# Kernel optimization log

Hardware: AMD Instinct MI355X
Metric: run time of the kernel (lower is better)

Reference implementation:

```python
import jax, jax.numpy as jnp
import numpy as np

B, S, D, H = 2, 2048, 1024, 16
HD = D // H  # head_dim = 64

def setup_inputs() -> dict:
    key = jax.random.key(0)
    ks = jax.random.split(key, 5)
    scale = 0.02
    return {
        "x":  jax.random.normal(ks[0], (B, S, D), dtype=jnp.float32),
        "Wq": jax.random.normal(ks[1], (D, D), dtype=jnp.float32) * scale,
        "Wk": jax.random.normal(ks[2], (D, D), dtype=jnp.float32) * scale,
        "Wv": jax.random.normal(ks[3], (D, D), dtype=jnp.float32) * scale,
        "Wo": jax.random.normal(ks[4], (D, D), dtype=jnp.float32) * scale,
    }

def reference(x, Wq, Wk, Wv, Wo):
    b, s, d = x.shape
    # projections (bias-free linear): [b,s,d] @ [d,d]
    q = (x @ Wq).reshape(b, s, H, HD).transpose(0, 2, 1, 3)  # [b,h,s,hd]
    k = (x @ Wk).reshape(b, s, H, HD).transpose(0, 2, 1, 3)
    v = (x @ Wv).reshape(b, s, H, HD).transpose(0, 2, 1, 3)
    scale = jnp.asarray(1.0 / np.sqrt(HD), dtype=x.dtype)
    scores = jnp.einsum('bhqd,bhkd->bhqk', q, k) * scale  # [b,h,s,s]
    causal = jnp.tril(jnp.ones((s, s), dtype=bool))
    scores = jnp.where(causal, scores, jnp.asarray(-jnp.inf, dtype=scores.dtype))
    attn = jax.nn.softmax(scores, axis=-1)
    out = jnp.einsum('bhqk,bhkd->bhqd', attn, v)  # [b,h,s,hd]
    out = out.transpose(0, 2, 1, 3).reshape(b, s, d)
    return out @ Wo
```

## Files before the change

kernel.cpp:

```cpp
#include <hip/hip_runtime.h>
#include <hip/hip_bf16.h>
#include <cstdint>

typedef __bf16 bf16;
typedef bf16 bf16x8 __attribute__((ext_vector_type(8)));
typedef bf16 bf16x4 __attribute__((ext_vector_type(4)));
typedef float f32x4 __attribute__((ext_vector_type(4)));

#define MFMA16(a, b, c) __builtin_amdgcn_mfma_f32_16x16x32_bf16(a, b, c, 0, 0, 0)

struct rawF { f32x4 a, b; };
__device__ inline rawF ldr(const float* p) {
  rawF r; r.a = *(const f32x4*)p; r.b = *(const f32x4*)(p + 4); return r;
}
__device__ inline bf16x8 ldr(const bf16* p) { return *(const bf16x8*)p; }
__device__ inline bf16x8 cv(const rawF& r) {
  bf16x8 o;
#pragma unroll
  for (int i = 0; i < 4; ++i) { o[i] = (bf16)r.a[i]; o[i + 4] = (bf16)r.b[i]; }
  return o;
}
__device__ inline bf16x8 cv(const bf16x8& r) { return r; }
__device__ inline void stC(bf16* C, size_t i, float v) { C[i] = (bf16)v; }
__device__ inline void stC(float* C, size_t i, float v) { C[i] = v; }

__global__ __launch_bounds__(256) void prep_wt(const float* __restrict__ W0,
                                               const float* __restrict__ W1,
                                               const float* __restrict__ W2,
                                               const float* __restrict__ W3,
                                               bf16* __restrict__ Wt, int n) {
  const float* Ws[4] = {W0, W1, W2, W3};
  const float* W = Ws[blockIdx.z];
  bf16* out = Wt + (size_t)blockIdx.z * n * n;
  __shared__ bf16 t[32][33];
  int bx = blockIdx.x * 32, by = blockIdx.y * 32;
  int tx = threadIdx.x & 31, ty = threadIdx.x >> 5;
#pragma unroll
  for (int i = 0; i < 32; i += 8)
    t[ty + i][tx] = (bf16)W[(size_t)(by + ty + i) * n + bx + tx];
  __syncthreads();
#pragma unroll
  for (int i = 0; i < 32; i += 8)
    out[(size_t)(bx + ty + i) * n + by + tx] = t[tx][ty + i];
}

__global__ __launch_bounds__(256) void vtrans(const bf16* __restrict__ V, bf16* __restrict__ Vt) {
  constexpr int Sn = 2048, Dn = 1024;
  __shared__ bf16 t[32][33];
  int s0 = blockIdx.x * 32, hd0 = blockIdx.y * 32, bh = blockIdx.z;
  int b = bh >> 4, h = bh & 15;
  int tx = threadIdx.x & 31, ty = threadIdx.x >> 5;
#pragma unroll
  for (int i = 0; i < 32; i += 8)
    t[ty + i][tx] = V[(size_t)(b * Sn + s0 + ty + i) * Dn + h * 64 + hd0 + tx];
  __syncthreads();
#pragma unroll
  for (int i = 0; i < 32; i += 8)
    Vt[(size_t)bh * 64 * Sn + (size_t)(hd0 + ty + i) * Sn + s0 + tx] = t[tx][ty + i];
}

template <typename TA, typename TC, bool BT>
__global__ __launch_bounds__(256) void gemm3(const TA* __restrict__ A,
                                             const void* __restrict__ B0p,
                                             const void* __restrict__ B1p,
                                             const void* __restrict__ B2p,
                                             TC* __restrict__ C0, TC* __restrict__ C1,
                                             TC* __restrict__ C2, int M, int N, int K, int nblk) {
  constexpr int LDA = 40;
  constexpr int LDB = BT ? 40 : 32;
  __shared__ bf16 As[128 * LDA];
  __shared__ bf16 Bs[128 * LDB];
  int tid = threadIdx.x, wave = tid >> 6, lane = tid & 63;
  int la = lane & 15, quad = lane >> 4;
  int wr = (wave >> 1) * 64, wc = (wave & 1) * 64;
  int by = blockIdx.y;
  int sel = by / nblk;
  int n0 = (by - sel * nblk) * 128;
  const void* Bp = sel == 0 ? B0p : (sel == 1 ? B1p : B2p);
  TC* C = sel == 0 ? C0 : (sel == 1 ? C1 : C2);
  const TA* Ab = A + (size_t)blockIdx.x * 128 * K;
  using TB = typename std::conditional<BT, bf16, float>::type;
  const TB* Bm = (const TB*)Bp;

  int ar[2], ac[2], br[2], bc[2];
#pragma unroll
  for (int p = 0; p < 2; ++p) {
    int li = (tid + p * 256) * 8;
    ar[p] = li >> 5; ac[p] = li & 31;
    if (BT) { br[p] = li >> 5; bc[p] = li & 31; }
    else    { br[p] = li >> 7; bc[p] = li & 127; }
  }

  f32x4 zero = {0.f, 0.f, 0.f, 0.f};
  f32x4 acc[4][4];
#pragma unroll
  for (int i = 0; i < 4; ++i)
#pragma unroll
    for (int j = 0; j < 4; ++j) acc[i][j] = zero;

  decltype(ldr((const TA*)nullptr)) pa[2];
  decltype(ldr((const TB*)nullptr)) pb[2];
#pragma unroll
  for (int p = 0; p < 2; ++p) {
    pa[p] = ldr(&Ab[(size_t)ar[p] * K + ac[p]]);
    if (BT) pb[p] = ldr(&Bm[(size_t)(n0 + br[p]) * K + bc[p]]);
    else    pb[p] = ldr(&Bm[(size_t)br[p] * N + n0 + bc[p]]);
  }

  for (int k0 = 0; k0 < K; k0 += 32) {
#pragma unroll
    for (int p = 0; p < 2; ++p) {
      *(bf16x8*)&As[ar[p] * LDA + ac[p]] = cv(pa[p]);
      if constexpr (BT) {
        *(bf16x8*)&Bs[br[p] * LDB + bc[p]] = cv(pb[p]);
      } else {
        bf16x8 v = cv(pb[p]);
        int kx = br[p] ^ (((bc[p] >> 3) & 3) << 3);
#pragma unroll
        for (int j = 0; j < 8; ++j) Bs[(bc[p] + j) * 32 + kx] = v[j];
      }
    }
    __syncthreads();
    int k1 = k0 + 32;
    if (k1 < K) {
#pragma unroll
      for (int p = 0; p < 2; ++p) {
        pa[p] = ldr(&Ab[(size_t)ar[p] * K + k1 + ac[p]]);
        if (BT) pb[p] = ldr(&Bm[(size_t)(n0 + br[p]) * K + k1 + bc[p]]);
        else    pb[p] = ldr(&Bm[(size_t)(k1 + br[p]) * N + n0 + bc[p]]);
      }
    }
    bf16x8 af[4], bfr[4];
#pragma unroll
    for (int i = 0; i < 4; ++i)
      af[i] = *(const bf16x8*)&As[(wr + i * 16 + la) * LDA + quad * 8];
#pragma unroll
    for (int j = 0; j < 4; ++j) {
      int nr = wc + j * 16 + la;
      if constexpr (BT)
        bfr[j] = *(const bf16x8*)&Bs[nr * LDB + quad * 8];
      else
        bfr[j] = *(const bf16x8*)&Bs[nr * 32 + ((quad * 8) ^ (((nr >> 3) & 3) << 3))];
    }
#pragma unroll
    for (int i = 0; i < 4; ++i)
#pragma unroll
      for (int j = 0; j < 4; ++j) acc[i][j] = MFMA16(af[i], bfr[j], acc[i][j]);
    __syncthreads();
  }
#pragma unroll
  for (int i = 0; i < 4; ++i) {
#pragma unroll
    for (int j = 0; j < 4; ++j) {
      int col = n0 + wc + j * 16 + la;
#pragma unroll
      for (int r = 0; r < 4; ++r) {
        int row = blockIdx.x * 128 + wr + i * 16 + quad * 4 + r;
        stC(C, (size_t)row * N + col, acc[i][j][r]);
      }
    }
  }
}

__global__ __launch_bounds__(256) void flash_attn(const bf16* __restrict__ Q,
                                                  const bf16* __restrict__ Kg,
                                                  const bf16* __restrict__ Vtg,
                                                  bf16* __restrict__ O) {
  constexpr int D = 1024, S = 2048;
  const int LDK = 72, LDP = 72;
  const float MASK = -3.0e4f;
  const float SCL2 = 0.18033688011112042f;
  __shared__ bf16 Ks[64 * 72];
  __shared__ bf16 Vs[64 * 72];
  __shared__ bf16 Ps[4][16 * 72];

  int n = blockIdx.x;
  int bh = n & 31;
  int j5 = n >> 5;
  int j = j5 & 15;
  int qt = (j5 & 16) ? 31 - j : j;
  int b = bh >> 4, h = bh & 15;
  int tid = threadIdx.x, wave = tid >> 6, lane = tid & 63;
  int la = lane & 15, quad = lane >> 4;
  const size_t base = (size_t)b * S * D + (size_t)h * 64;
  const bf16* Qg = Q + base;
  const bf16* Kb = Kg + base;
  const bf16* Vb = Vtg + (size_t)bh * 64 * S;
  int r0 = tid >> 3, c0 = (tid & 7) * 8;

  f32x4 zero = {0.f, 0.f, 0.f, 0.f};

  int q0 = qt * 64;
  int ntiles = qt + 1;

  bf16x8 aq[2];
  {
    int qrow = q0 + wave * 16 + la;
#pragma unroll
    for (int kc = 0; kc < 2; ++kc) {
      bf16x8 t = *(const bf16x8*)&Qg[(size_t)qrow * D + kc * 32 + quad * 8];
#pragma unroll
      for (int i = 0; i < 8; ++i) t[i] = (bf16)((float)t[i] * SCL2);
      aq[kc] = t;
    }
  }

  f32x4 o[4];
#pragma unroll
  for (int nt = 0; nt < 4; ++nt) o[nt] = zero;
  float m_l = MASK, l_l = 0.f;

  bf16x8 kr0 = *(const bf16x8*)&Kb[(size_t)r0 * D + c0];
  bf16x8 kr1 = *(const bf16x8*)&Kb[(size_t)(r0 + 32) * D + c0];
  bf16x8 vr0 = *(const bf16x8*)&Vb[(size_t)r0 * S + c0];
  bf16x8 vr1 = *(const bf16x8*)&Vb[(size_t)(r0 + 32) * S + c0];

  for (int t = 0; t < ntiles; ++t) {
    int kb = t * 64;
    *(bf16x8*)&Ks[r0 * LDK + c0] = kr0;
    *(bf16x8*)&Ks[(r0 + 32) * LDK + c0] = kr1;
    *(bf16x8*)&Vs[r0 * LDK + c0] = vr0;
    *(bf16x8*)&Vs[(r0 + 32) * LDK + c0] = vr1;
    __syncthreads();
    if (t + 1 < ntiles) {
      int kb2 = kb + 64;
      kr0 = *(const bf16x8*)&Kb[(size_t)(kb2 + r0) * D + c0];
      kr1 = *(const bf16x8*)&Kb[(size_t)(kb2 + r0 + 32) * D + c0];
      vr0 = *(const bf16x8*)&Vb[(size_t)r0 * S + kb2 + c0];
      vr1 = *(const bf16x8*)&Vb[(size_t)(r0 + 32) * S + kb2 + c0];
    }

    f32x4 s[4];
    __builtin_amdgcn_s_setprio(1);
#pragma unroll
    for (int nt = 0; nt < 4; ++nt) {
      bf16x8 k0f = *(const bf16x8*)&Ks[(nt * 16 + la) * LDK + quad * 8];
      bf16x8 k1f = *(const bf16x8*)&Ks[(nt * 16 + la) * LDK + 32 + quad * 8];
      f32x4 z = zero;
      z = MFMA16(k0f, aq[0], z);
      z = MFMA16(k1f, aq[1], z);
      s[nt] = z;
    }
    __builtin_amdgcn_s_setprio(0);

    if (t == qt) {
      int qa = q0 + wave * 16 + la;
#pragma unroll
      for (int nt = 0; nt < 4; ++nt)
#pragma unroll
        for (int r = 0; r < 4; ++r) {
          int ka = kb + nt * 16 + quad * 4 + r;
          s[nt][r] = (ka > qa) ? MASK : s[nt][r];
        }
    }

    float mx;
    {
      float t0 = fmaxf(fmaxf(s[0][0], s[0][1]), fmaxf(s[0][2], s[0][3]));
      float t1 = fmaxf(fmaxf(s[1][0], s[1][1]), fmaxf(s[1][2], s[1][3]));
      float t2 = fmaxf(fmaxf(s[2][0], s[2][1]), fmaxf(s[2][2], s[2][3]));
      float t3 = fmaxf(fmaxf(s[3][0], s[3][1]), fmaxf(s[3][2], s[3][3]));
      mx = fmaxf(fmaxf(t0, t1), fmaxf(t2, t3));
    }
    mx = fmaxf(mx, m_l);
    mx = fmaxf(mx, __shfl_xor(mx, 16, 64));
    mx = fmaxf(mx, __shfl_xor(mx, 32, 64));

    if (!__all(mx - m_l <= 8.0f)) {
      float alpha = __builtin_amdgcn_exp2f(m_l - mx);
      m_l = mx;
      l_l *= alpha;
      float ab[4];
#pragma unroll
      for (int r = 0; r < 4; ++r) ab[r] = __shfl(alpha, quad * 4 + r, 64);
#pragma unroll
      for (int nt = 0; nt < 4; ++nt)
#pragma unroll
        for (int r = 0; r < 4; ++r) o[nt][r] *= ab[r];
    }

    float rs = 0.f;
#pragma unroll
    for (int nt = 0; nt < 4; ++nt) {
      float p0 = __builtin_amdgcn_exp2f(s[nt][0] - m_l);
      float p1 = __builtin_amdgcn_exp2f(s[nt][1] - m_l);
      float p2 = __builtin_amdgcn_exp2f(s[nt][2] - m_l);
      float p3 = __builtin_amdgcn_exp2f(s[nt][3] - m_l);
      s[nt][0] = p0; s[nt][1] = p1; s[nt][2] = p2; s[nt][3] = p3;
      rs += (p0 + p1) + (p2 + p3);
    }
    rs += __shfl_xor(rs, 16, 64);
    rs += __shfl_xor(rs, 32, 64);
    l_l += rs;

#pragma unroll
    for (int nt = 0; nt < 4; ++nt) {
      bf16x4 pk;
#pragma unroll
      for (int r = 0; r < 4; ++r) pk[r] = (bf16)s[nt][r];
      *(bf16x4*)&Ps[wave][la * LDP + nt * 16 + quad * 4] = pk;
    }

    __builtin_amdgcn_s_setprio(1);
#pragma unroll
    for (int kc = 0; kc < 2; ++kc) {
      bf16x8 ap = *(const bf16x8*)&Ps[wave][la * LDP + kc * 32 + quad * 8];
#pragma unroll
      for (int nt = 0; nt < 4; ++nt) {
        bf16x8 bv = *(const bf16x8*)&Vs[(nt * 16 + la) * LDK + kc * 32 + quad * 8];
        o[nt] = MFMA16(ap, bv, o[nt]);
      }
    }
    __builtin_amdgcn_s_setprio(0);
    __syncthreads();
  }

  float inv[4];
#pragma unroll
  for (int r = 0; r < 4; ++r) {
    float lv = __shfl(l_l, quad * 4 + r, 64);
    inv[r] = (lv > 1e-30f) ? 1.0f / lv : 0.0f;
  }
#pragma unroll
  for (int nt = 0; nt < 4; ++nt) {
    int hd = nt * 16 + la;
#pragma unroll
    for (int r = 0; r < 4; ++r) {
      int row = q0 + wave * 16 + quad * 4 + r;
      O[base + (size_t)row * D + hd] = (bf16)(o[nt][r] * inv[r]);
    }
  }
}

extern "C" void kernel_launch(void* const* d_in, const int* in_sizes, int n_in,
                              void* d_out, int out_size, void* d_ws, size_t ws_size,
                              hipStream_t stream) {
  constexpr int B = 2, S = 2048, D = 1024;
  constexpr int M = B * S;
  constexpr size_t WN = (size_t)D * D;
  constexpr size_t XN = (size_t)M * D;

  const float* x = (const float*)d_in[0];
  const float* Wq = (const float*)d_in[1];
  const float* Wk = (const float*)d_in[2];
  const float* Wv = (const float*)d_in[3];
  const float* Wo = (const float*)d_in[4];
  float* out = (float*)d_out;

  if (ws_size < 2 * XN * sizeof(bf16)) return;
  bf16* Qb = (bf16*)d_ws;
  bf16* Vtg = Qb + XN;
  bf16* Wt = Vtg + XN;
  bf16* Kb = (bf16*)d_out;
  bf16* Vb = Kb + XN;
  bool use_bt = ws_size >= (2 * XN + 4 * WN) * sizeof(bf16);

  dim3 gq(M / 128, 24), gf(M / 128, 8);
  if (use_bt) {
    prep_wt<<<dim3(32, 32, 4), 256, 0, stream>>>(Wq, Wk, Wv, Wo, Wt, D);
    gemm3<float, bf16, true><<<gq, 256, 0, stream>>>(x, Wt, Wt + WN, Wt + 2 * WN,
                                                     Qb, Kb, Vb, M, D, D, 8);
  } else {
    gemm3<float, bf16, false><<<gq, 256, 0, stream>>>(x, Wq, Wk, Wv, Qb, Kb, Vb, M, D, D, 8);
  }
  vtrans<<<dim3(S / 32, 2, 32), 256, 0, stream>>>(Vb, Vtg);
  flash_attn<<<dim3(1024), 256, 0, stream>>>(Qb, Kb, Vtg, Qb);
  if (use_bt) {
    gemm3<bf16, float, true><<<gf, 256, 0, stream>>>(Qb, Wt + 3 * WN, Wt + 3 * WN, Wt + 3 * WN,
                                                     out, out, out, M, D, D, 8);
  } else {
    gemm3<bf16, float, false><<<gf, 256, 0, stream>>>(Qb, Wo, Wo, Wo, out, out, out, M, D, D, 8);
  }
}
```

Measured before the change: 182.7 us.

## Split long causal attention rows across two blocks and swizzle LDS layout

The 15 longest query tiles per head now have their KV range split between two blocks. The first block to finish writes its partial O, m and l to scratch and the second merges them through an atomic flag handshake. The aim is to even out the causal load imbalance and fill the GPU better with 1504 blocks. LDS tiles also move from padded rows to an XOR-swizzled layout to avoid bank conflicts. The change adds a memset launch, scratch traffic and a spin-wait, and it relies on both halves being co-resident so the spin cannot deadlock.

New measurement: 351.6 us. 1.92x slower.

```diff
diff --git a/kernel.cpp b/kernel.cpp
--- a/kernel.cpp
+++ b/kernel.cpp
@@ -165,20 +165,38 @@
 __global__ __launch_bounds__(256) void flash_attn(const bf16* __restrict__ Q,
                                                   const bf16* __restrict__ Kg,
                                                   const bf16* __restrict__ Vtg,
-                                                  bf16* __restrict__ O) {
+                                                  bf16* __restrict__ O,
+                                                  float* __restrict__ PO,
+                                                  float* __restrict__ Pm,
+                                                  float* __restrict__ Pl,
+                                                  unsigned* __restrict__ Pf) {
   constexpr int D = 1024, S = 2048;
-  const int LDK = 72, LDP = 72;
   const float MASK = -3.0e4f;
   const float SCL2 = 0.18033688011112042f;
-  __shared__ bf16 Ks[64 * 72];
-  __shared__ bf16 Vs[64 * 72];
-  __shared__ bf16 Ps[4][16 * 72];
+  __shared__ bf16 Ks[4096];
+  __shared__ bf16 Vs[4096];
+  __shared__ bf16 Ps[4096];
+  __shared__ int roleShare;
 
   int n = blockIdx.x;
   int bh = n & 31;
-  int j5 = n >> 5;
-  int j = j5 & 15;
-  int qt = (j5 & 16) ? 31 - j : j;
+  int it = n >> 5;
+  int qt, t0, t1, pa_ = 0;
+  bool split;
+  if (it < 30) {
+    pa_ = it >> 1;
+    int half = it & 1;
+    qt = 31 - pa_;
+    int hsp = (qt + 1) >> 1;
+    split = true;
+    t0 = half ? hsp : 0;
+    t1 = half ? qt + 1 : hsp;
+  } else {
+    qt = 46 - it;
+    split = false;
+    t0 = 0;
+    t1 = qt + 1;
+  }
   int b = bh >> 4, h = bh & 15;
   int tid = threadIdx.x, wave = tid >> 6, lane = tid & 63;
   int la = lane & 15, quad = lane >> 4;
@@ -188,10 +206,18 @@
   const bf16* Vb = Vtg + (size_t)bh * 64 * S;
   int r0 = tid >> 3, c0 = (tid & 7) * 8;
 
+  int quads = (tid & 7) & 3, kcs = (tid & 7) >> 2;
+  int st0 = (r0 >> 4) * 1024 + kcs * 512 + quads * 128 +
+            (((r0 & 15) ^ quads ^ (kcs << 2)) * 8);
+  int kvrd0 = quad * 128 + ((la ^ quad) * 8);
+  int kvrd1 = 512 + quad * 128 + ((la ^ quad ^ 4) * 8);
+  int prd0 = wave * 1024 + quad * 128 + ((la ^ ((quad & 1) << 2)) * 8);
+  int prd1 = prd0 + 512;
+  int pwb = wave * 1024 + (quad >> 1) * 128 +
+            ((la ^ ((quad >> 1) << 2)) * 8) + (quad & 1) * 4;
+
   f32x4 zero = {0.f, 0.f, 0.f, 0.f};
-
   int q0 = qt * 64;
-  int ntiles = qt + 1;
 
   bf16x8 aq[2];
   {
@@ -210,20 +236,20 @@
   for (int nt = 0; nt < 4; ++nt) o[nt] = zero;
   float m_l = MASK, l_l = 0.f;
 
-  bf16x8 kr0 = *(const bf16x8*)&Kb[(size_t)r0 * D + c0];
-  bf16x8 kr1 = *(const bf16x8*)&Kb[(size_t)(r0 + 32) * D + c0];
-  bf16x8 vr0 = *(const bf16x8*)&Vb[(size_t)r0 * S + c0];
-  bf16x8 vr1 = *(const bf16x8*)&Vb[(size_t)(r0 + 32) * S + c0];
-
-  for (int t = 0; t < ntiles; ++t) {
-    int kb = t * 64;
-    *(bf16x8*)&Ks[r0 * LDK + c0] = kr0;
-    *(bf16x8*)&Ks[(r0 + 32) * LDK + c0] = kr1;
-    *(bf16x8*)&Vs[r0 * LDK + c0] = vr0;
-    *(bf16x8*)&Vs[(r0 + 32) * LDK + c0] = vr1;
-    __syncthreads();
-    if (t + 1 < ntiles) {
-      int kb2 = kb + 64;
+  int kb0 = t0 * 64;
+  bf16x8 kr0 = *(const bf16x8*)&Kb[(size_t)(kb0 + r0) * D + c0];
+  bf16x8 kr1 = *(const bf16x8*)&Kb[(size_t)(kb0 + r0 + 32) * D + c0];
+  bf16x8 vr0 = *(const bf16x8*)&Vb[(size_t)r0 * S + kb0 + c0];
+  bf16x8 vr1 = *(const bf16x8*)&Vb[(size_t)(r0 + 32) * S + kb0 + c0];
+
+  for (int t = t0; t < t1; ++t) {
+    *(bf16x8*)&Ks[st0] = kr0;
+    *(bf16x8*)&Ks[st0 + 2048] = kr1;
+    *(bf16x8*)&Vs[st0] = vr0;
+    *(bf16x8*)&Vs[st0 + 2048] = vr1;
+    __syncthreads();
+    if (t + 1 < t1) {
+      int kb2 = (t + 1) * 64;
       kr0 = *(const bf16x8*)&Kb[(size_t)(kb2 + r0) * D + c0];
       kr1 = *(const bf16x8*)&Kb[(size_t)(kb2 + r0 + 32) * D + c0];
       vr0 = *(const bf16x8*)&Vb[(size_t)r0 * S + kb2 + c0];
@@ -234,8 +260,8 @@
     __builtin_amdgcn_s_setprio(1);
 #pragma unroll
     for (int nt = 0; nt < 4; ++nt) {
-      bf16x8 k0f = *(const bf16x8*)&Ks[(nt * 16 + la) * LDK + quad * 8];
-      bf16x8 k1f = *(const bf16x8*)&Ks[(nt * 16 + la) * LDK + 32 + quad * 8];
+      bf16x8 k0f = *(const bf16x8*)&Ks[nt * 1024 + kvrd0];
+      bf16x8 k1f = *(const bf16x8*)&Ks[nt * 1024 + kvrd1];
       f32x4 z = zero;
       z = MFMA16(k0f, aq[0], z);
       z = MFMA16(k1f, aq[1], z);
@@ -245,6 +271,7 @@
 
     if (t == qt) {
       int qa = q0 + wave * 16 + la;
+      int kb = t * 64;
 #pragma unroll
       for (int nt = 0; nt < 4; ++nt)
 #pragma unroll
@@ -256,11 +283,11 @@
 
     float mx;
     {
-      float t0 = fmaxf(fmaxf(s[0][0], s[0][1]), fmaxf(s[0][2], s[0][3]));
-      float t1 = fmaxf(fmaxf(s[1][0], s[1][1]), fmaxf(s[1][2], s[1][3]));
-      float t2 = fmaxf(fmaxf(s[2][0], s[2][1]), fmaxf(s[2][2], s[2][3]));
-      float t3 = fmaxf(fmaxf(s[3][0], s[3][1]), fmaxf(s[3][2], s[3][3]));
-      mx = fmaxf(fmaxf(t0, t1), fmaxf(t2, t3));
+      float u0 = fmaxf(fmaxf(s[0][0], s[0][1]), fmaxf(s[0][2], s[0][3]));
+      float u1 = fmaxf(fmaxf(s[1][0], s[1][1]), fmaxf(s[1][2], s[1][3]));
+      float u2 = fmaxf(fmaxf(s[2][0], s[2][1]), fmaxf(s[2][2], s[2][3]));
+      float u3 = fmaxf(fmaxf(s[3][0], s[3][1]), fmaxf(s[3][2], s[3][3]));
+      mx = fmaxf(fmaxf(u0, u1), fmaxf(u2, u3));
     }
     mx = fmaxf(mx, m_l);
     mx = fmaxf(mx, __shfl_xor(mx, 16, 64));
@@ -298,36 +325,99 @@
       bf16x4 pk;
 #pragma unroll
       for (int r = 0; r < 4; ++r) pk[r] = (bf16)s[nt][r];
-      *(bf16x4*)&Ps[wave][la * LDP + nt * 16 + quad * 4] = pk;
+      *(bf16x4*)&Ps[pwb + nt * 256] = pk;
     }
 
     __builtin_amdgcn_s_setprio(1);
-#pragma unroll
-    for (int kc = 0; kc < 2; ++kc) {
-      bf16x8 ap = *(const bf16x8*)&Ps[wave][la * LDP + kc * 32 + quad * 8];
+    {
+      bf16x8 ap0 = *(const bf16x8*)&Ps[prd0];
 #pragma unroll
       for (int nt = 0; nt < 4; ++nt) {
-        bf16x8 bv = *(const bf16x8*)&Vs[(nt * 16 + la) * LDK + kc * 32 + quad * 8];
-        o[nt] = MFMA16(ap, bv, o[nt]);
+        bf16x8 bv = *(const bf16x8*)&Vs[nt * 1024 + kvrd0];
+        o[nt] = MFMA16(ap0, bv, o[nt]);
+      }
+      bf16x8 ap1 = *(const bf16x8*)&Ps[prd1];
+#pragma unroll
+      for (int nt = 0; nt < 4; ++nt) {
+        bf16x8 bv = *(const bf16x8*)&Vs[nt * 1024 + kvrd1];
+        o[nt] = MFMA16(ap1, bv, o[nt]);
       }
     }
     __builtin_amdgcn_s_setprio(0);
     __syncthreads();
   }
 
-  float inv[4];
+  if (!split) {
+    float inv[4];
+#pragma unroll
+    for (int r = 0; r < 4; ++r) {
+      float lv = __shfl(l_l, quad * 4 + r, 64);
+      inv[r] = (lv > 1e-30f) ? 1.0f / lv : 0.0f;
+    }
+#pragma unroll
+    for (int nt = 0; nt < 4; ++nt) {
+      int hd = nt * 16 + la;
+#pragma unroll
+      for (int r = 0; r < 4; ++r) {
+        int row = q0 + wave * 16 + quad * 4 + r;
+        O[base + (size_t)row * D + hd] = (bf16)(o[nt][r] * inv[r]);
+      }
+    }
+    return;
+  }
+
+  int pidx = pa_ * 32 + bh;
+  float* myO = PO + (size_t)pidx * 4096;
+  if (tid == 0)
+    roleShare = (int)__hip_atomic_fetch_add(&Pf[pidx], 1u, __ATOMIC_ACQ_REL,
+                                            __HIP_MEMORY_SCOPE_AGENT);
+  __syncthreads();
+  int role = roleShare;
+  if (role == 0) {
+#pragma unroll
+    for (int nt = 0; nt < 4; ++nt)
+#pragma unroll
+      for (int r = 0; r < 4; ++r)
+        myO[(wave * 16 + quad * 4 + r) * 64 + nt * 16 + la] = o[nt][r];
+    if (quad == 0) {
+      Pm[pidx * 64 + wave * 16 + la] = m_l;
+      Pl[pidx * 64 + wave * 16 + la] = l_l;
+    }
+    __threadfence();
+    __syncthreads();
+    if (tid == 0)
+      __hip_atomic_fetch_add(&Pf[pidx], 1u, __ATOMIC_RELEASE, __HIP_MEMORY_SCOPE_AGENT);
+    return;
+  }
+  if (role == 1) {
+    if (tid == 0) {
+      while (__hip_atomic_load(&Pf[pidx], __ATOMIC_ACQUIRE, __HIP_MEMORY_SCOPE_AGENT) < 3u) {}
+    }
+    __syncthreads();
+  }
+  __threadfence();
+  float m2 = Pm[pidx * 64 + wave * 16 + la];
+  float l2 = Pl[pidx * 64 + wave * 16 + la];
+  float mM = fmaxf(m_l, m2);
+  float a1 = __builtin_amdgcn_exp2f(m_l - mM);
+  float a2 = __builtin_amdgcn_exp2f(m2 - mM);
+  float lM = l_l * a1 + l2 * a2;
+  float linv = (lM > 1e-30f) ? 1.0f / lM : 0.0f;
+  float a1b[4], a2b[4], ivb[4];
 #pragma unroll
   for (int r = 0; r < 4; ++r) {
-    float lv = __shfl(l_l, quad * 4 + r, 64);
-    inv[r] = (lv > 1e-30f) ? 1.0f / lv : 0.0f;
+    a1b[r] = __shfl(a1, quad * 4 + r, 64);
+    a2b[r] = __shfl(a2, quad * 4 + r, 64);
+    ivb[r] = __shfl(linv, quad * 4 + r, 64);
   }
 #pragma unroll
   for (int nt = 0; nt < 4; ++nt) {
     int hd = nt * 16 + la;
 #pragma unroll
     for (int r = 0; r < 4; ++r) {
+      float o2 = myO[(wave * 16 + quad * 4 + r) * 64 + hd];
       int row = q0 + wave * 16 + quad * 4 + r;
-      O[base + (size_t)row * D + hd] = (bf16)(o[nt][r] * inv[r]);
+      O[base + (size_t)row * D + hd] = (bf16)((o[nt][r] * a1b[r] + o2 * a2b[r]) * ivb[r]);
     }
   }
 }
@@ -355,6 +445,12 @@
   bf16* Vb = Kb + XN;
   bool use_bt = ws_size >= (2 * XN + 4 * WN) * sizeof(bf16);
 
+  char* pbase = (char*)d_out + XN * sizeof(bf16);
+  float* PO = (float*)pbase;
+  float* Pm = PO + 480 * 4096;
+  float* Pl = Pm + 480 * 64;
+  unsigned* Pf = (unsigned*)(Pl + 480 * 64);
+
   dim3 gq(M / 128, 24), gf(M / 128, 8);
   if (use_bt) {
     prep_wt<<<dim3(32, 32, 4), 256, 0, stream>>>(Wq, Wk, Wv, Wo, Wt, D);
@@ -364,7 +460,8 @@
     gemm3<float, bf16, false><<<gq, 256, 0, stream>>>(x, Wq, Wk, Wv, Qb, Kb, Vb, M, D, D, 8);
   }
   vtrans<<<dim3(S / 32, 2, 32), 256, 0, stream>>>(Vb, Vtg);
-  flash_attn<<<dim3(1024), 256, 0, stream>>>(Qb, Kb, Vtg, Qb);
+  hipMemsetAsync(Pf, 0, 480 * sizeof(unsigned), stream);
+  flash_attn<<<dim3(1504), 256, 0, stream>>>(Qb, Kb, Vtg, Qb, PO, Pm, Pl, Pf);
   if (use_bt) {
     gemm3<bf16, float, true><<<gf, 256, 0, stream>>>(Qb, Wt + 3 * WN, Wt + 3 * WN, Wt + 3 * WN,
                                                      out, out, out, M, D, D, 8);
```
